# Performance work log

Measured on AMD Instinct MI355X. Metric: run time of the kernel, lower is better.

Reference implementation:

```python
import jax, jax.numpy as jnp
import numpy as np

NEG = jnp.float32(-1e30)  # log(0) surrogate


def _ctc_loss(logits, labels, label_lengths):
    """CTC loss matching tf.nn.ctc_loss semantics: softmax applied internally,
    blank index = last class, full logit_length = T, mean over batch.

    logits: [B, T, C] float, labels: [B, L] int (padded), label_lengths: [B] int.
    """
    B, T, C = logits.shape
    blank = C - 1
    logp = jax.nn.log_softmax(logits.astype(jnp.float32), axis=-1)  # [B,T,C]
    L = labels.shape[1]
    S = 2 * L + 1  # extended label: blank, l1, blank, l2, ..., blank

    ext = jnp.full((B, S), blank, dtype=jnp.int32).at[:, 1::2].set(labels.astype(jnp.int32))
    # emission log-probs per extended position: [B, T, S]
    emit = jnp.take_along_axis(logp, jnp.broadcast_to(ext[:, None, :], (B, T, S)), axis=2)

    # skip transition s-2 -> s allowed iff ext[s] is a label differing from ext[s-2]
    prev2 = jnp.pad(ext[:, :-2], ((0, 0), (2, 0)), constant_values=-1)
    allow2 = (ext != blank) & (ext != prev2)  # [B,S]

    ll = label_lengths.astype(jnp.int32)
    valid = jnp.arange(S)[None, :] < (2 * ll[:, None] + 1)  # [B,S]

    # t = 0: only s=0 (blank) and s=1 (first label) reachable
    alpha0 = jnp.full((B, S), NEG)
    alpha0 = alpha0.at[:, 0].set(0.0)
    alpha0 = alpha0.at[:, 1].set(jnp.where(ll > 0, 0.0, NEG))
    alpha0 = jnp.where(valid, alpha0 + emit[:, 0, :], NEG)

    def step(alpha, emit_t):
        s1 = jnp.pad(alpha[:, :-1], ((0, 0), (1, 0)), constant_values=NEG)
        s2 = jnp.pad(alpha[:, :-2], ((0, 0), (2, 0)), constant_values=NEG)
        s2 = jnp.where(allow2, s2, NEG)
        a = jax.scipy.special.logsumexp(jnp.stack([alpha, s1, s2]), axis=0) + emit_t
        a = jnp.where(valid, a, NEG)
        return a, None

    alpha, _ = jax.lax.scan(step, alpha0, jnp.swapaxes(emit, 0, 1)[1:])  # scan over T-1 steps

    # terminate at final blank (s=2*ll) or final label (s=2*ll-1)
    a_end1 = jnp.take_along_axis(alpha, (2 * ll)[:, None], axis=1)[:, 0]
    a_end2 = jnp.take_along_axis(alpha, jnp.maximum(2 * ll - 1, 0)[:, None], axis=1)[:, 0]
    a_end2 = jnp.where(ll > 0, a_end2, NEG)
    loss = -jnp.logaddexp(a_end1, a_end2)  # [B]
    return jnp.mean(loss)


def setup_inputs() -> dict:
    key = jax.random.key(0)
    k1, k2, k3 = jax.random.split(key, 3)
    B, T, L, C = 32, 1024, 128, 801  # C = num_classes + 1 (blank = 800)
    logits = jax.random.normal(k1, (B, T, C), dtype=jnp.float32)
    labels = jax.random.randint(k2, (B, L), 0, 800, dtype=jnp.int32)
    label_lengths = jax.random.randint(k3, (B,), 64, L + 1, dtype=jnp.int32)
    return {"logits": logits, "labels": labels, "label_lengths": label_lengths}


def reference(logits, labels, label_lengths):
    return _ctc_loss(logits, labels, label_lengths)
```

## Files before the change

### kernel.cpp

```cpp
#include <hip/hip_runtime.h>
#include <math.h>

#define B_ 32
#define T_ 1024
#define C_ 801
#define L_ 128
#define S_ 257
#define BLANK 800
#define NEGV -1e30f

#define CH 128
#define NCH (T_ / CH)
#define NW 8
#define LN2F 0.69314718055994531f

typedef const unsigned __attribute__((address_space(1))) u32_g;
typedef unsigned __attribute__((address_space(3))) u32_l;

template <int CTRL>
__device__ __forceinline__ float dppf(float v) {
    return __uint_as_float((unsigned)__builtin_amdgcn_update_dpp(
        0, (int)__float_as_uint(v), CTRL, 0xf, 0xf, true));
}
__device__ __forceinline__ float shift_up1(float v) { return dppf<0x138>(v); }

__device__ __forceinline__ float wave_red_max63(float v) {
    v = fmaxf(v, dppf<0xB1>(v));
    v = fmaxf(v, dppf<0x4E>(v));
    v = fmaxf(v, dppf<0x141>(v));
    v = fmaxf(v, dppf<0x140>(v));
    v = fmaxf(v, dppf<0x142>(v));
    v = fmaxf(v, dppf<0x143>(v));
    return v;
}
__device__ __forceinline__ float wave_red_sum63(float v) {
    v += dppf<0xB1>(v);
    v += dppf<0x4E>(v);
    v += dppf<0x141>(v);
    v += dppf<0x140>(v);
    v += dppf<0x142>(v);
    v += dppf<0x143>(v);
    return v;
}
__device__ __forceinline__ float bcast63(float v) {
    return __uint_as_float((unsigned)__builtin_amdgcn_readlane((int)__float_as_uint(v), 63));
}
__device__ __forceinline__ float wave_max_nn(float v) { return bcast63(wave_red_max63(v)); }

__device__ __forceinline__ float bf16lo(unsigned u) { return __uint_as_float(u << 16); }
__device__ __forceinline__ float bf16hi(unsigned u) { return __uint_as_float(u & 0xFFFF0000u); }
__device__ __forceinline__ unsigned short f32_to_bf16_rne(float f) {
    unsigned u = __float_as_uint(f);
    u += 0x7FFF + ((u >> 16) & 1);
    return (unsigned short)(u >> 16);
}

#define RLANE(x, j) __uint_as_float((unsigned)__builtin_amdgcn_readlane((int)__float_as_uint(x), (j)))

__global__ __launch_bounds__(256) void stage_kernel(const float* __restrict__ logits,
                                                    const int* __restrict__ labels,
                                                    const int* __restrict__ lens,
                                                    unsigned* __restrict__ ea32,
                                                    float* __restrict__ ebq) {
    const int tid = threadIdx.x, lane = tid & 63, wv = tid >> 6;
    const int b = blockIdx.y;
    const int t0 = blockIdx.x * 4;
    const float* __restrict__ base = logits + ((size_t)b * T_ + t0) * C_;
    __shared__ float xs[4 * C_];

    const float4* src = (const float4*)base;
    #pragma unroll
    for (int k = 0; k < 4; ++k) {
        int idx = tid + 256 * k;
        if (idx < 801) ((float4*)xs)[idx] = src[idx];
    }
    __syncthreads();

    const float* xr = xs + wv * C_;
    float v[13];
    #pragma unroll
    for (int k = 0; k < 12; ++k) v[k] = xr[lane + 64 * k];
    v[12] = (lane < 33) ? xr[768 + lane] : NEGV;

    float s = 0.f;
    #pragma unroll
    for (int k = 0; k < 13; ++k) s += __expf(v[k]);
    s = bcast63(wave_red_sum63(s));
    const float lse = __logf(s);

    const int ll = lens[b];
    const int row = b * T_ + (t0 + wv);
    const float ebl = __expf(xr[BLANK] - lse) * 1024.0f;
    const int cls1 = labels[b * L_ + 2 * lane];
    const int cls3 = labels[b * L_ + 2 * lane + 1];
    float e1 = (2 * lane     < ll) ? __expf(xr[cls1] - lse) * 1024.0f : 0.f;
    float e3 = (2 * lane + 1 < ll) ? __expf(xr[cls3] - lse) * 1024.0f : 0.f;

    unsigned pack = ((unsigned)f32_to_bf16_rne(e3) << 16) | (unsigned)f32_to_bf16_rne(e1);
    ea32[(size_t)row * 64 + lane] = pack;
    if (lane == 0) ebq[row] = ebl;
}


__device__ __forceinline__ void stage_chunk_split(const unsigned* gbase, int c,
                                                  unsigned* lbase, int lane, int wid) {
    #pragma unroll
    for (int k = 0; k < CH / NW; ++k) {
        int r = wid + k * NW;
        const unsigned* gp = gbase + ((size_t)(c * CH + r)) * 64 + lane;
        unsigned* lp = lbase + r * 64;
        __builtin_amdgcn_global_load_lds((u32_g*)gp, (u32_l*)lp, 4, 0, 0);
    }
}

template <int FIRST>
__device__ __forceinline__ void compute_chunk(const unsigned* bufp, float ebv0, float ebv1,
                                              int lane, float m21, float m23,
                                              float& p0, float& p1, float& p2, float& p3,
                                              float& q, int& E) {
    #pragma unroll
    for (int g = 0; g < CH / 8; ++g) {
        unsigned u[8];
        #pragma unroll
        for (int k = 0; k < 8; ++k) u[k] = bufp[(g * 8 + k) * 64 + lane];
        #pragma unroll
        for (int k = 0; k < 8; ++k) {
            if (FIRST && g == 0 && k == 0) continue;
            const int j = g * 8 + k;
            float ebt = (j < 64) ? RLANE(ebv0, j) : RLANE(ebv1, j - 64);
            float el0 = bf16lo(u[k]);
            float el1 = bf16hi(u[k]);
            float shp3 = shift_up1(p3);
            float n0 = (p0 + shp3) * ebt;
            float n1 = fmaf(m21, shp3, p1 + p0) * el0;
            float n2 = (p2 + p1) * ebt;
            float n3 = fmaf(m23, p1, p3 + p2) * el1;
            q = (q + p3) * ebt;
            p0 = n0; p1 = n1; p2 = n2; p3 = n3;
        }
        float mx = fmaxf(fmaxf(p0, p1), fmaxf(p2, fmaxf(p3, q)));
        mx = wave_max_nn(mx);
        int e2_ = (int)((__float_as_uint(mx) >> 23) & 0xFF) - 126;
        float sc_ = __uint_as_float((unsigned)(127 - e2_) << 23);
        p0 *= sc_; p1 *= sc_; p2 *= sc_; p3 *= sc_; q *= sc_;
        E += e2_;
    }
}

__global__ __launch_bounds__(NW * 64) void ctc_lds_kernel(const unsigned* __restrict__ ea32,
                                                          const float* __restrict__ ebq,
                                                          const int* __restrict__ labels,
                                                          const int* __restrict__ lens,
                                                          float* __restrict__ out) {
    __shared__ unsigned buf[2][CH * 64];
    const int b = blockIdx.x;
    const int tid = threadIdx.x;
    const int lane = tid & 63;
    const int wid = tid >> 6;
    const int ll = lens[b];
    const unsigned* gbase = ea32 + (size_t)b * T_ * 64;
    const float* qb = ebq + b * T_;

    float m21 = 0.f, m23 = 0.f;
    if (wid == 0) {
        int s1 = 4 * lane + 1;
        if (s1 >= 3) {
            int li = s1 >> 1;
            m21 = (labels[b * L_ + li] != labels[b * L_ + li - 1]) ? 1.f : 0.f;
        }
        int li3 = (4 * lane + 3) >> 1;
        m23 = (labels[b * L_ + li3] != labels[b * L_ + li3 - 1]) ? 1.f : 0.f;
    }

    stage_chunk_split(gbase, 0, buf[0], lane, wid);
    float ebv0 = 0.f, ebv1 = 0.f, ebn0 = 0.f, ebn1 = 0.f;
    if (wid == 0) { ebv0 = qb[lane]; ebv1 = qb[64 + lane]; }
    __syncthreads();

    float p0 = 0.f, p1 = 0.f, p2 = 0.f, p3 = 0.f, q = 0.f;
    if (wid == 0) {
        float eb0 = RLANE(ebv0, 0);
        unsigned w0 = buf[0][lane];
        p0 = (lane == 0) ? eb0 : 0.f;
        p1 = (lane == 0) ? bf16lo(w0) : 0.f;
    }
    int E = 0;

    #pragma unroll 1
    for (int c = 0; c < NCH; ++c) {
        if (c + 1 < NCH) {
            stage_chunk_split(gbase, c + 1, buf[(c + 1) & 1], lane, wid);
            if (wid == 0) { ebn0 = qb[(c + 1) * CH + lane]; ebn1 = qb[(c + 1) * CH + 64 + lane]; }
        }
        if (wid == 0) {
            if (c == 0) compute_chunk<1>(buf[0],     ebv0, ebv1, lane, m21, m23,
                                         p0, p1, p2, p3, q, E);
            else        compute_chunk<0>(buf[c & 1], ebv0, ebv1, lane, m21, m23,
                                         p0, p1, p2, p3, q, E);
            ebv0 = ebn0; ebv1 = ebn1;
        }
        __syncthreads();
    }

    float* pf = (float*)(&buf[0][0]);
    if (wid == 0) {
        *(float4*)(pf + 4 * lane) = make_float4(p0, p1, p2, p3);
        if (lane == 63) pf[256] = q;
    }
    __syncthreads();
    if (tid == 0) {
        float a1 = pf[2 * ll];
        float a2 = (ll > 0) ? pf[2 * ll - 1] : 0.f;
        float l = -(__logf(a1 + a2) + ((float)E - 10240.0f) * LN2F);
        atomicAdd(out, l * (1.0f / (float)B_));
    }
}

__global__ void mean_kernel(const float* __restrict__ loss, float* __restrict__ out) {
    if (threadIdx.x == 0) {
        float s = 0.f;
        for (int i = 0; i < B_; ++i) s += loss[i];
        out[0] = s / (float)B_;
    }
}


__global__ __launch_bounds__(256) void lse_kernel(const float* __restrict__ logits,
                                                  float* __restrict__ lse) {
    const int row = blockIdx.x;
    const float* __restrict__ x = logits + (size_t)row * C_;
    const int tid = threadIdx.x, lane = tid & 63, wid = tid >> 6;
    float v0 = x[tid], v1 = x[tid + 256], v2 = x[tid + 512];
    bool h3 = (tid + 768) < C_;
    float v3 = h3 ? x[tid + 768] : NEGV;
    float m = fmaxf(fmaxf(v0, v1), fmaxf(v2, v3));
    #pragma unroll
    for (int off = 32; off > 0; off >>= 1) m = fmaxf(m, __shfl_down(m, off));
    __shared__ float wred[4]; __shared__ float bm;
    if (lane == 0) wred[wid] = m;
    __syncthreads();
    if (tid == 0) bm = fmaxf(fmaxf(wred[0], wred[1]), fmaxf(wred[2], wred[3]));
    __syncthreads();
    m = bm;
    float s = __expf(v0 - m) + __expf(v1 - m) + __expf(v2 - m);
    if (h3) s += __expf(v3 - m);
    #pragma unroll
    for (int off = 32; off > 0; off >>= 1) s += __shfl_down(s, off);
    __syncthreads();
    if (lane == 0) wred[wid] = s;
    __syncthreads();
    if (tid == 0) lse[row] = m + __logf(wred[0] + wred[1] + wred[2] + wred[3]);
}

__global__ __launch_bounds__(320) void ctc_alpha_kernel(const float* __restrict__ logits,
                                                        const int* __restrict__ labels,
                                                        const int* __restrict__ lens,
                                                        const float* __restrict__ lse,
                                                        float* __restrict__ loss) {
    const int b = blockIdx.x;
    const int s = threadIdx.x;
    const int ll = lens[b];
    __shared__ float albuf[2][S_ + 2];
    if (s < 2) { albuf[0][s] = NEGV; albuf[1][s] = NEGV; }
    int cls = BLANK; bool allow2 = false;
    if (s < S_ && (s & 1)) {
        cls = labels[b * L_ + (s >> 1)];
        allow2 = (s >= 3) && (cls != labels[b * L_ + (s >> 1) - 1]);
    }
    const bool valid = (s < 2 * ll + 1);
    const float* __restrict__ xb = logits + (size_t)b * T_ * C_;
    const float* __restrict__ lseb = lse + b * T_;
    if (s < S_) {
        float e0 = xb[cls] - lseb[0];
        float a = (s == 0 || (s == 1 && ll > 0)) ? e0 : NEGV;
        if (!valid) a = NEGV;
        albuf[0][2 + s] = a;
    }
    __syncthreads();
    float e_next = xb[(size_t)C_ + cls];
    float lse_next = lseb[1];
    int cur = 0;
    for (int t = 1; t < T_; ++t) {
        const float e = e_next, lse_t = lse_next;
        if (t + 1 < T_) { e_next = xb[(size_t)(t + 1) * C_ + cls]; lse_next = lseb[t + 1]; }
        if (s < S_) {
            float a0 = albuf[cur][2 + s];
            float a1 = albuf[cur][1 + s];
            float a2 = allow2 ? albuf[cur][s] : NEGV;
            float m = fmaxf(fmaxf(a0, a1), a2);
            float r = m + __logf(__expf(a0 - m) + __expf(a1 - m) + __expf(a2 - m)) + (e - lse_t);
            if (!valid) r = NEGV;
            albuf[cur ^ 1][2 + s] = r;
        }
        __syncthreads();
        cur ^= 1;
    }
    if (s == 0) {
        float a1 = albuf[cur][2 + 2 * ll];
        float a2 = (ll > 0) ? albuf[cur][2 + 2 * ll - 1] : NEGV;
        float m = fmaxf(a1, a2);
        loss[b] = -(m + __logf(__expf(a1 - m) + __expf(a2 - m)));
    }
}


extern "C" void kernel_launch(void* const* d_in, const int* in_sizes, int n_in,
                              void* d_out, int out_size, void* d_ws, size_t ws_size,
                              hipStream_t stream) {
    const float* logits = (const float*)d_in[0];
    const int*   labels = (const int*)d_in[1];
    const int*   lens   = (const int*)d_in[2];
    float* out = (float*)d_out;

    const size_t ea_elems = (size_t)B_ * T_ * 64;
    const size_t eb_elems = (size_t)B_ * T_;
    const size_t need = (ea_elems + eb_elems) * 4;

    if (ws_size >= need) {
        unsigned* ea32 = (unsigned*)d_ws;
        float* ebq = (float*)(ea32 + ea_elems);
        hipMemsetAsync(out, 0, sizeof(float), stream);
        dim3 grid(T_ / 4, B_);
        stage_kernel<<<grid, 256, 0, stream>>>(logits, labels, lens, ea32, ebq);
        ctc_lds_kernel<<<B_, NW * 64, 0, stream>>>(ea32, ebq, labels, lens, out);
    } else {
        float* lse  = (float*)d_ws;
        float* loss = lse + (size_t)B_ * T_;
        lse_kernel<<<B_ * T_, 256, 0, stream>>>(logits, lse);
        ctc_alpha_kernel<<<B_, 320, 0, stream>>>(logits, labels, lens, lse, loss);
        mean_kernel<<<1, 64, 0, stream>>>(loss, out);
    }
}
```

Before: 73.87 us.

## Factor blank emission out of CTC recurrence and accumulate its log separately

The preprocessing now stores label emissions as ratios relative to the blank emission, so the serial alpha recurrence no longer multiplies every state by the per-timestep blank probability. Removing that factor also drops the cross-lane broadcast of the blank value from the critical loop. A second wave sums log(blank prob) over time in parallel, and that total is added back to the final loss. The serial dependency chain gets shorter, at the cost of extra log work in a side wave and a possible precision change from storing ratios in bf16.

```diff
diff --git a/kernel.cpp b/kernel.cpp
--- a/kernel.cpp
+++ b/kernel.cpp
@@ -90,15 +90,15 @@
 
     const int ll = lens[b];
     const int row = b * T_ + (t0 + wv);
-    const float ebl = __expf(xr[BLANK] - lse) * 1024.0f;
+    const float xbl = xr[BLANK];
     const int cls1 = labels[b * L_ + 2 * lane];
     const int cls3 = labels[b * L_ + 2 * lane + 1];
-    float e1 = (2 * lane     < ll) ? __expf(xr[cls1] - lse) * 1024.0f : 0.f;
-    float e3 = (2 * lane + 1 < ll) ? __expf(xr[cls3] - lse) * 1024.0f : 0.f;
-
-    unsigned pack = ((unsigned)f32_to_bf16_rne(e3) << 16) | (unsigned)f32_to_bf16_rne(e1);
+    float r1 = (2 * lane     < ll) ? __expf(xr[cls1] - xbl) : 0.f;
+    float r3 = (2 * lane + 1 < ll) ? __expf(xr[cls3] - xbl) : 0.f;
+
+    unsigned pack = ((unsigned)f32_to_bf16_rne(r3) << 16) | (unsigned)f32_to_bf16_rne(r1);
     ea32[(size_t)row * 64 + lane] = pack;
-    if (lane == 0) ebq[row] = ebl;
+    if (lane == 0) ebq[row] = __expf(xbl - lse) * 1024.0f;
 }
 
 
@@ -114,8 +114,8 @@
 }
 
 template <int FIRST>
-__device__ __forceinline__ void compute_chunk(const unsigned* bufp, float ebv0, float ebv1,
-                                              int lane, float m21, float m23,
+__device__ __forceinline__ void compute_chunk(const unsigned* bufp, int lane,
+                                              float m21, float m23,
                                               float& p0, float& p1, float& p2, float& p3,
                                               float& q, int& E) {
     #pragma unroll
@@ -126,16 +126,14 @@
         #pragma unroll
         for (int k = 0; k < 8; ++k) {
             if (FIRST && g == 0 && k == 0) continue;
-            const int j = g * 8 + k;
-            float ebt = (j < 64) ? RLANE(ebv0, j) : RLANE(ebv1, j - 64);
-            float el0 = bf16lo(u[k]);
-            float el1 = bf16hi(u[k]);
+            float r0 = bf16lo(u[k]);
+            float r1 = bf16hi(u[k]);
             float shp3 = shift_up1(p3);
-            float n0 = (p0 + shp3) * ebt;
-            float n1 = fmaf(m21, shp3, p1 + p0) * el0;
-            float n2 = (p2 + p1) * ebt;
-            float n3 = fmaf(m23, p1, p3 + p2) * el1;
-            q = (q + p3) * ebt;
+            float n0 = p0 + shp3;
+            float n1 = fmaf(m21, shp3, p1 + p0) * r0;
+            float n2 = p2 + p1;
+            float n3 = fmaf(m23, p1, p3 + p2) * r1;
+            q = q + p3;
             p0 = n0; p1 = n1; p2 = n2; p3 = n3;
         }
         float mx = fmaxf(fmaxf(p0, p1), fmaxf(p2, fmaxf(p3, q)));
@@ -153,6 +151,7 @@
                                                           const int* __restrict__ lens,
                                                           float* __restrict__ out) {
     __shared__ unsigned buf[2][CH * 64];
+    __shared__ float Dsh;
     const int b = blockIdx.x;
     const int tid = threadIdx.x;
     const int lane = tid & 63;
@@ -173,31 +172,30 @@
     }
 
     stage_chunk_split(gbase, 0, buf[0], lane, wid);
-    float ebv0 = 0.f, ebv1 = 0.f, ebn0 = 0.f, ebn1 = 0.f;
-    if (wid == 0) { ebv0 = qb[lane]; ebv1 = qb[64 + lane]; }
     __syncthreads();
 
     float p0 = 0.f, p1 = 0.f, p2 = 0.f, p3 = 0.f, q = 0.f;
     if (wid == 0) {
-        float eb0 = RLANE(ebv0, 0);
+        float eb0 = qb[0];
         unsigned w0 = buf[0][lane];
         p0 = (lane == 0) ? eb0 : 0.f;
-        p1 = (lane == 0) ? bf16lo(w0) : 0.f;
+        p1 = (lane == 0) ? bf16lo(w0) * eb0 : 0.f;
     }
     int E = 0;
+    float Dacc = 0.f;
 
     #pragma unroll 1
     for (int c = 0; c < NCH; ++c) {
-        if (c + 1 < NCH) {
-            stage_chunk_split(gbase, c + 1, buf[(c + 1) & 1], lane, wid);
-            if (wid == 0) { ebn0 = qb[(c + 1) * CH + lane]; ebn1 = qb[(c + 1) * CH + 64 + lane]; }
-        }
+        if (c + 1 < NCH) stage_chunk_split(gbase, c + 1, buf[(c + 1) & 1], lane, wid);
         if (wid == 0) {
-            if (c == 0) compute_chunk<1>(buf[0],     ebv0, ebv1, lane, m21, m23,
-                                         p0, p1, p2, p3, q, E);
-            else        compute_chunk<0>(buf[c & 1], ebv0, ebv1, lane, m21, m23,
-                                         p0, p1, p2, p3, q, E);
-            ebv0 = ebn0; ebv1 = ebn1;
+            if (c == 0) compute_chunk<1>(buf[0],     lane, m21, m23, p0, p1, p2, p3, q, E);
+            else        compute_chunk<0>(buf[c & 1], lane, m21, m23, p0, p1, p2, p3, q, E);
+        } else if (wid == 1) {
+            float q0 = qb[c * CH + lane];
+            float q1 = qb[c * CH + 64 + lane];
+            float l0 = __logf(q0), l1 = __logf(q1);
+            if (c == 0 && lane == 0) l0 = 0.f;
+            Dacc += l0 + l1;
         }
         __syncthreads();
     }
@@ -206,12 +204,15 @@
     if (wid == 0) {
         *(float4*)(pf + 4 * lane) = make_float4(p0, p1, p2, p3);
         if (lane == 63) pf[256] = q;
+    } else if (wid == 1) {
+        float Dtot = wave_red_sum63(Dacc);
+        if (lane == 63) Dsh = Dtot;
     }
     __syncthreads();
     if (tid == 0) {
         float a1 = pf[2 * ll];
         float a2 = (ll > 0) ? pf[2 * ll - 1] : 0.f;
-        float l = -(__logf(a1 + a2) + ((float)E - 10240.0f) * LN2F);
+        float l = -(__logf(a1 + a2) + Dsh + ((float)E - 10240.0f) * LN2F);
         atomicAdd(out, l * (1.0f / (float)B_));
     }
 }
```

After: 68.41 us. 1.08x faster.
